# Performance work log

Hardware: AMD Instinct MI355X
Metric: run time of the kernel (lower is better)

Reference implementation:

```python
import jax, jax.numpy as jnp
import numpy as np


def setup_inputs() -> dict:
    key = jax.random.key(0)
    k1, k2 = jax.random.split(key)
    B, H, W, D, C = 2, 128, 128, 128, 4
    image = jax.random.normal(k1, (B, H, W, D, C), dtype=jnp.float32)
    # multiplicative warp field in [0,1) keeps sample coords inside the volume
    transformation = jax.random.uniform(k2, (B, H, W, D, 3), dtype=jnp.float32)
    return {"image": image, "transformation": transformation}


def _make_grid(OH, OW, OD):
    # matches tf.meshgrid(x_lin, y_lin, z_lin) with default 'xy' indexing:
    # each output has shape (OH, OW, OD); stacked last-dim order (x, y, z)
    xl = jnp.linspace(-1.0, 1.0, OW)
    yl = jnp.linspace(-1.0, 1.0, OH)
    zl = jnp.linspace(-1.0, 1.0, OD)
    xc, yc, zc = jnp.meshgrid(xl, yl, zl, indexing="xy")
    return jnp.stack([xc, yc, zc], axis=-1)  # (OH, OW, OD, 3)


def _trilerp_one(img, coords):
    """img: (H, W, D, C); coords: (OH, OW, OD, 3) in [-1, 1]-style space."""
    H, W, D, C = img.shape
    x = 0.5 * (coords[..., 0] + 1.0) * W
    y = 0.5 * (coords[..., 1] + 1.0) * H
    z = 0.5 * (coords[..., 2] + 1.0) * D

    x0 = jnp.floor(x).astype(jnp.int32)
    y0 = jnp.floor(y).astype(jnp.int32)
    z0 = jnp.floor(z).astype(jnp.int32)
    x1 = jnp.clip(x0 + 1, 0, W - 1)
    y1 = jnp.clip(y0 + 1, 0, H - 1)
    z1 = jnp.clip(z0 + 1, 0, D - 1)
    x0 = jnp.clip(x0, 0, W - 1)
    y0 = jnp.clip(y0, 0, H - 1)
    z0 = jnp.clip(z0, 0, D - 1)

    # weights use the CLIPPED upper corners, as in the original
    dx = x1.astype(x.dtype) - x
    dy = y1.astype(y.dtype) - y
    dz = z1.astype(z.dtype) - z

    def g(yy, xx, zz):
        return img[yy, xx, zz]  # (OH, OW, OD, C) gather

    w = lambda a: a[..., None]
    out = (
        w(dz * dx * dy) * g(y0, x0, z0)
        + w(dz * dx * (1 - dy)) * g(y1, x0, z0)
        + w(dz * (1 - dx) * dy) * g(y0, x1, z0)
        + w(dz * (1 - dx) * (1 - dy)) * g(y1, x1, z0)
        + w((1 - dz) * dx * dy) * g(y0, x0, z1)
        + w((1 - dz) * dx * (1 - dy)) * g(y1, x0, z1)
        + w((1 - dz) * (1 - dx) * dy) * g(y0, x1, z1)
        + w((1 - dz) * (1 - dx) * (1 - dy)) * g(y1, x1, z1)
    )
    return out


def reference(image, transformation):
    # image: (B, H, W, D, C); transformation: (B, OH, OW, OD, 3)
    OH, OW, OD = transformation.shape[1:4]
    grid = _make_grid(OH, OW, OD)              # (OH, OW, OD, 3)
    coords = transformation * grid             # elementwise warp, as in source
    return jax.vmap(_trilerp_one, in_axes=(0, 0))(image, coords)
```

## Files before the change

kernel.cpp:

```cpp
#include <hip/hip_runtime.h>
#include <hip/hip_fp16.h>


typedef float f4 __attribute__((ext_vector_type(4)));
typedef unsigned int u32;
typedef u32 u4v __attribute__((ext_vector_type(4), aligned(8)));

__device__ inline float2 h2f(u32 b) {
    __half2 h = __builtin_bit_cast(__half2, b);
    return __half22float2(h);
}
__device__ inline u32 f2h2(float a, float b) {
    __half2 h = __floats2half2_rn(a, b);
    return __builtin_bit_cast(u32, h);
}

__global__ __launch_bounds__(256) void cvtq_kernel(
    const f4* __restrict__ img, u4v* __restrict__ rec, int bb)
{
    int t = blockIdx.x * 256 + threadIdx.x;
    int z = t & 127;
    int x = (t >> 7) & 127;
    int y = t >> 14;
    int x1 = min(x + 1, 127);
    int y1 = min(y + 1, 127);

    f4 v00 = img[bb | (y  << 14) | (x  << 7) | z];
    f4 v10 = img[bb | (y1 << 14) | (x  << 7) | z];
    f4 v01 = img[bb | (y  << 14) | (x1 << 7) | z];
    f4 v11 = img[bb | (y1 << 14) | (x1 << 7) | z];

    int tt = bb | t;

    u4v r0 = { f2h2(v00.x, v00.y), f2h2(v00.z, v00.w),
               f2h2(v10.x, v10.y), f2h2(v10.z, v10.w) };
    u4v r1 = { f2h2(v01.x, v01.y), f2h2(v01.z, v01.w),
               f2h2(v11.x, v11.y), f2h2(v11.z, v11.w) };
    rec[(size_t)tt * 2]     = r0;
    rec[(size_t)tt * 2 + 1] = r1;
}

__global__ __launch_bounds__(256) void st3d_q_kernel(
    const u32* __restrict__ rec,
    const float* __restrict__ trans,
    f4* __restrict__ out,
    int bb)
{
    int bid = blockIdx.x;
    int q   = bid & 7;
    int n   = bid >> 3;
    int mA  = (n << 8) | threadIdx.x;
    int mB  = mA + (1 << 17);

    int qi = (q >> 2) & 1;
    int qj = (q >> 1) & 1;
    int qk = q & 1;

    const float step = 2.0f / 127.0f;

#define SETUPQ(S, mval)                                                    \
    int kp##S  = (mval) & 63;                                              \
    int jp##S  = ((mval) >> 6) & 63;                                       \
    int ip##S  = (mval) >> 12;                                             \
    int ipe##S = qi ? ip##S : (63 - ip##S);      \
    int i##S   = (qi << 6) + ipe##S;                                       \
    int j##S   = (qj << 6) + jp##S;                                        \
    int k##S   = (qk << 6) + kp##S;                                        \
    int idx##S = bb | (i##S << 14) | (j##S << 7) | k##S;                   \
    const float* t##S = trans + (size_t)idx##S * 3;                        \
    float tx##S = __builtin_nontemporal_load(t##S + 0);                    \
    float ty##S = __builtin_nontemporal_load(t##S + 1);                    \
    float tz##S = __builtin_nontemporal_load(t##S + 2);

    SETUPQ(A, mA)
    SETUPQ(B, mB)

#define GATHERQ(S)                                                         \
    float gx##S = -1.0f + step * (float)j##S;                              \
    float gy##S = -1.0f + step * (float)i##S;                              \
    float gz##S = -1.0f + step * (float)k##S;                              \
    float x##S = (tx##S * gx##S + 1.0f) * 64.0f;                           \
    float y##S = (ty##S * gy##S + 1.0f) * 64.0f;                           \
    float z##S = (tz##S * gz##S + 1.0f) * 64.0f;                           \
    int x0##S = (int)floorf(x##S);                                         \
    int y0##S = (int)floorf(y##S);                                         \
    int z0##S = (int)floorf(z##S);                                         \
    int x1##S = min(max(x0##S + 1, 0), 127);                               \
    int y1##S = min(max(y0##S + 1, 0), 127);                               \
    int z1##S = min(max(z0##S + 1, 0), 127);                               \
    x0##S = min(max(x0##S, 0), 127);                                       \
    y0##S = min(max(y0##S, 0), 127);                                       \
    z0##S = min(max(z0##S, 0), 127);                                       \
              \
    float dx##S = (float)x1##S - x##S;                                     \
    float dy##S = (float)y1##S - y##S;                                     \
    float dz##S = (float)z1##S - z##S;                                     \
    int zb##S = min(z0##S, 126);            \
    int i0##S = z0##S - zb##S;             \
    int i1##S = z1##S - zb##S;                             \
    int r##S = bb | (y0##S << 14) | (x0##S << 7) | zb##S;                  \
    const u4v* p##S = (const u4v*)(rec + (size_t)r##S * 8);                \
    u4v L0##S = p##S[0];                       \
    u4v L1##S = p##S[1];                       \
    u4v L2##S = p##S[2];                       \
    u4v L3##S = p##S[3];

    GATHERQ(A)
    GATHERQ(B)

#define ACCQ(lo0, lo1, hi0, hi1, wA, wB)                                   \
    {                                                                      \
        u32 a0 = i0s ? (hi0) : (lo0);                       \
        u32 a1 = i0s ? (hi1) : (lo1);                       \
        u32 b0 = i1s ? (hi0) : (lo0);                       \
        u32 b1 = i1s ? (hi1) : (lo1);                       \
        float2 fa0 = h2f(a0), fa1 = h2f(a1);                               \
        float2 fb0 = h2f(b0), fb1 = h2f(b1);                               \
        ox += (wA) * fa0.x + (wB) * fb0.x;                                 \
        oy += (wA) * fa0.y + (wB) * fb0.y;                                 \
        oz += (wA) * fa1.x + (wB) * fb1.x;                                 \
        ow += (wA) * fa1.y + (wB) * fb1.y;                                 \
    }

#define FINISHQ(S)                                                         \
    {                                                                      \
        float ex = 1.0f - dx##S, ey = 1.0f - dy##S, ez = 1.0f - dz##S;     \
        float wA0 = dz##S * dx##S * dy##S, wB0 = ez * dx##S * dy##S;       \
        float wA1 = dz##S * dx##S * ey,    wB1 = ez * dx##S * ey;          \
        float wA2 = dz##S * ex * dy##S,    wB2 = ez * ex * dy##S;          \
        float wA3 = dz##S * ex * ey,       wB3 = ez * ex * ey;             \
        int i0s = i0##S, i1s = i1##S;                                      \
        float ox = 0.f, oy = 0.f, oz = 0.f, ow = 0.f;                      \
        ACCQ(L0##S.x, L0##S.y, L2##S.x, L2##S.y, wA0, wB0)    \
        ACCQ(L0##S.z, L0##S.w, L2##S.z, L2##S.w, wA1, wB1)    \
        ACCQ(L1##S.x, L1##S.y, L3##S.x, L3##S.y, wA2, wB2)    \
        ACCQ(L1##S.z, L1##S.w, L3##S.z, L3##S.w, wA3, wB3)    \
        f4 o = {ox, oy, oz, ow};                                           \
        __builtin_nontemporal_store(o, &out[idx##S]);                      \
    }

    FINISHQ(A)
    FINISHQ(B)

#undef SETUPQ
#undef GATHERQ
#undef ACCQ
#undef FINISHQ
}

__global__ __launch_bounds__(256) void cvt_kernel(
    const f4* __restrict__ img, uint2* __restrict__ himg)
{
    int idx = blockIdx.x * 256 + threadIdx.x;
    f4 v = img[idx];
    __half2 lo = __floats2half2_rn(v.x, v.y);
    __half2 hi = __floats2half2_rn(v.z, v.w);
    himg[idx] = make_uint2(__builtin_bit_cast(u32, lo), __builtin_bit_cast(u32, hi));
}

__global__ __launch_bounds__(256) void st3d_h_kernel(
    const u32* __restrict__ himg,
    const float* __restrict__ trans,
    f4* __restrict__ out)
{
    int bid = blockIdx.x;
    int q   = bid & 7;
    int n   = bid >> 3;
    int b   = n >> 10;
    int m   = ((n & 1023) << 8) | threadIdx.x;

    int kp = m & 63;
    int jp = (m >> 6) & 63;
    int ip = m >> 12;

    int qi = (q >> 2) & 1;
    int qj = (q >> 1) & 1;
    int qk = q & 1;

    int ipe = qi ? ip : (63 - ip);
    int i = (qi << 6) + ipe;
    int j = (qj << 6) + jp;
    int k = (qk << 6) + kp;

    int idx = (((b << 7) | i) << 14) | (j << 7) | k;

    const float step = 2.0f / 127.0f;
    float gx = -1.0f + step * (float)j;
    float gy = -1.0f + step * (float)i;
    float gz = -1.0f + step * (float)k;

    const float* t = trans + (size_t)idx * 3;
    float tx = __builtin_nontemporal_load(t + 0);
    float ty = __builtin_nontemporal_load(t + 1);
    float tz = __builtin_nontemporal_load(t + 2);

    float x = (tx * gx + 1.0f) * 64.0f;
    float y = (ty * gy + 1.0f) * 64.0f;
    float z = (tz * gz + 1.0f) * 64.0f;

    int x0 = (int)floorf(x);
    int y0 = (int)floorf(y);
    int z0 = (int)floorf(z);
    int x1 = min(max(x0 + 1, 0), 127);
    int y1 = min(max(y0 + 1, 0), 127);
    int z1 = min(max(z0 + 1, 0), 127);
    x0 = min(max(x0, 0), 127);
    y0 = min(max(y0, 0), 127);
    z0 = min(max(z0, 0), 127);

    float dx = (float)x1 - x;
    float dy = (float)y1 - y;
    float dz = (float)z1 - z;
    float ex = 1.0f - dx;
    float ey = 1.0f - dy;
    float ez = 1.0f - dz;

    int zb = min(z0, 126);
    int i0 = z0 - zb;
    int i1 = z1 - zb;

    int bb  = b << 21;
    int ry0 = bb + (y0 << 14);
    int ry1 = bb + (y1 << 14);
    int cx0 = x0 << 7;
    int cx1 = x1 << 7;

    const u4v* p0 = (const u4v*)(himg + (size_t)(ry0 + cx0 + zb) * 2);
    const u4v* p1 = (const u4v*)(himg + (size_t)(ry1 + cx0 + zb) * 2);
    const u4v* p2 = (const u4v*)(himg + (size_t)(ry0 + cx1 + zb) * 2);
    const u4v* p3 = (const u4v*)(himg + (size_t)(ry1 + cx1 + zb) * 2);

    u4v d0 = *p0;
    u4v d1 = *p1;
    u4v d2 = *p2;
    u4v d3 = *p3;

    float wA0 = dz * dx * dy, wB0 = ez * dx * dy;
    float wA1 = dz * dx * ey, wB1 = ez * dx * ey;
    float wA2 = dz * ex * dy, wB2 = ez * ex * dy;
    float wA3 = dz * ex * ey, wB3 = ez * ex * ey;

    float ox = 0.f, oy = 0.f, oz = 0.f, ow = 0.f;

#define ACC(d, wA, wB)                                            \
    {                                                             \
        u32 a0 = i0 ? (d).z : (d).x;                              \
        u32 a1 = i0 ? (d).w : (d).y;                              \
        u32 b0 = i1 ? (d).z : (d).x;                              \
        u32 b1 = i1 ? (d).w : (d).y;                              \
        float2 fa0 = h2f(a0), fa1 = h2f(a1);                      \
        float2 fb0 = h2f(b0), fb1 = h2f(b1);                      \
        ox += (wA) * fa0.x + (wB) * fb0.x;                        \
        oy += (wA) * fa0.y + (wB) * fb0.y;                        \
        oz += (wA) * fa1.x + (wB) * fb1.x;                        \
        ow += (wA) * fa1.y + (wB) * fb1.y;                        \
    }

    ACC(d0, wA0, wB0)
    ACC(d1, wA1, wB1)
    ACC(d2, wA2, wB2)
    ACC(d3, wA3, wB3)
#undef ACC

    f4 o = {ox, oy, oz, ow};
    __builtin_nontemporal_store(o, &out[idx]);
}

__global__ __launch_bounds__(256) void st3d_kernel(
    const float* __restrict__ img,
    const float* __restrict__ trans,
    f4* __restrict__ out)
{
    int bid = blockIdx.x;
    int q   = bid & 7;
    int n   = bid >> 3;
    int b   = n >> 10;
    int m   = ((n & 1023) << 8) | threadIdx.x;

    int kp = m & 63;
    int jp = (m >> 6) & 63;
    int ip = m >> 12;

    int qi = (q >> 2) & 1;
    int qj = (q >> 1) & 1;
    int qk = q & 1;

    int ipe = qi ? ip : (63 - ip);
    int i = (qi << 6) + ipe;
    int j = (qj << 6) + jp;
    int k = (qk << 6) + kp;

    int idx = (((b << 7) | i) << 14) | (j << 7) | k;

    const float step = 2.0f / 127.0f;
    float gx = -1.0f + step * (float)j;
    float gy = -1.0f + step * (float)i;
    float gz = -1.0f + step * (float)k;

    const float* t = trans + (size_t)idx * 3;
    float tx = __builtin_nontemporal_load(t + 0);
    float ty = __builtin_nontemporal_load(t + 1);
    float tz = __builtin_nontemporal_load(t + 2);

    float x = (tx * gx + 1.0f) * 64.0f;
    float y = (ty * gy + 1.0f) * 64.0f;
    float z = (tz * gz + 1.0f) * 64.0f;

    int x0 = (int)floorf(x);
    int y0 = (int)floorf(y);
    int z0 = (int)floorf(z);
    int x1 = min(max(x0 + 1, 0), 127);
    int y1 = min(max(y0 + 1, 0), 127);
    int z1 = min(max(z0 + 1, 0), 127);
    x0 = min(max(x0, 0), 127);
    y0 = min(max(y0, 0), 127);
    z0 = min(max(z0, 0), 127);

    float dx = (float)x1 - x;
    float dy = (float)y1 - y;
    float dz = (float)z1 - z;
    float ex = 1.0f - dx;
    float ey = 1.0f - dy;
    float ez = 1.0f - dz;

    const f4* img4 = (const f4*)img;
    int bb  = b << 21;
    int ry0 = bb + (y0 << 14);
    int ry1 = bb + (y1 << 14);
    int cx0 = x0 << 7;
    int cx1 = x1 << 7;

    int A0 = ry0 + cx0 + z0;
    int A1 = ry1 + cx0 + z0;
    int A2 = ry0 + cx1 + z0;
    int A3 = ry1 + cx1 + z0;
    int dzi = z1 - z0;

    f4 c000 = img4[A0];
    f4 c100 = img4[A1];
    f4 c010 = img4[A2];
    f4 c110 = img4[A3];
    f4 c001 = img4[A0 + dzi];
    f4 c101 = img4[A1 + dzi];
    f4 c011 = img4[A2 + dzi];
    f4 c111 = img4[A3 + dzi];

    float w000 = dz * dx * dy;
    float w100 = dz * dx * ey;
    float w010 = dz * ex * dy;
    float w110 = dz * ex * ey;
    float w001 = ez * dx * dy;
    float w101 = ez * dx * ey;
    float w011 = ez * ex * dy;
    float w111 = ez * ex * ey;

    f4 o = w000*c000 + w100*c100 + w010*c010 + w110*c110
         + w001*c001 + w101*c101 + w011*c011 + w111*c111;

    __builtin_nontemporal_store(o, &out[idx]);
}

extern "C" void kernel_launch(void* const* d_in, const int* in_sizes, int n_in,
                              void* d_out, int out_size, void* d_ws, size_t ws_size,
                              hipStream_t stream) {
    const float* img   = (const float*)d_in[0];
    const float* trans = (const float*)d_in[1];
    f4* out = (f4*)d_out;

    int N = in_sizes[1] / 3;
    int NB = 1 << 21;
    int block = 256;

    size_t need_q = (size_t)N * 32;
    size_t need_h = (size_t)N * 8;

    if (ws_size >= need_q) {
        for (int b = 0; b < 2; ++b) {
            int bb = b << 21;
            cvtq_kernel<<<NB / block, block, 0, stream>>>(
                (const f4*)img, (u4v*)d_ws, bb);
            st3d_q_kernel<<<NB / (2 * block), block, 0, stream>>>(
                (const u32*)d_ws, trans, out, bb);
        }
    } else if (ws_size >= need_h) {
        cvt_kernel<<<N / block, block, 0, stream>>>((const f4*)img, (uint2*)d_ws);
        st3d_h_kernel<<<N / block, block, 0, stream>>>(
            (const u32*)d_ws, trans, out);
    } else {
        st3d_kernel<<<N / block, block, 0, stream>>>(img, trans, out);
    }
}
```

Baseline: 227.9 us.

## Overlap batch-1 conversion with batch-0 sampling in an interleaved fused kernel

Replaces the per-batch sequence of conversion and sampling launches with three launches. The middle kernel interleaves batch-0 trilinear sampling blocks with batch-1 fp16 neighbour-record conversion blocks in a 1:2 ratio, so the memory-bound conversion overlaps the gather-heavy sampling. This removes one launch and one serialization point. The cost is more complex block indexing, and a mixed workload in one kernel may compete for bandwidth and cache.

```diff
diff --git a/kernel.cpp b/kernel.cpp
--- a/kernel.cpp
+++ b/kernel.cpp
@@ -15,10 +15,9 @@
     return __builtin_bit_cast(u32, h);
 }
 
-__global__ __launch_bounds__(256) void cvtq_kernel(
-    const f4* __restrict__ img, u4v* __restrict__ rec, int bb)
-{
-    int t = blockIdx.x * 256 + threadIdx.x;
+__device__ __forceinline__ void cvtq_body(
+    const f4* __restrict__ img, u4v* __restrict__ rec, int bb, int t)
+{
     int z = t & 127;
     int x = (t >> 7) & 127;
     int y = t >> 14;
@@ -40,16 +39,11 @@
     rec[(size_t)tt * 2 + 1] = r1;
 }
 
-__global__ __launch_bounds__(256) void st3d_q_kernel(
-    const u32* __restrict__ rec,
-    const float* __restrict__ trans,
-    f4* __restrict__ out,
-    int bb)
-{
-    int bid = blockIdx.x;
-    int q   = bid & 7;
-    int n   = bid >> 3;
-    int mA  = (n << 8) | threadIdx.x;
+__device__ __forceinline__ void st3d_q_body(
+    const u32* __restrict__ rec, const float* __restrict__ trans,
+    f4* __restrict__ out, int bb, int q, int n, int tid)
+{
+    int mA  = (n << 8) | tid;
     int mB  = mA + (1 << 17);
 
     int qi = (q >> 2) & 1;
@@ -148,6 +142,38 @@
 #undef FINISHQ
 }
 
+__global__ __launch_bounds__(256) void cvtq_kernel(
+    const f4* __restrict__ img, u4v* __restrict__ rec, int bb)
+{
+    cvtq_body(img, rec, bb, blockIdx.x * 256 + threadIdx.x);
+}
+
+__global__ __launch_bounds__(256) void fused_kernel(
+    const f4* __restrict__ img, u4v* __restrict__ rec_w,
+    const u32* __restrict__ rec, const float* __restrict__ trans,
+    f4* __restrict__ out)
+{
+    int bid = blockIdx.x;
+    int d3  = bid / 3;
+    int r3  = bid - d3 * 3;
+    if (r3 == 0) {
+        int q = bid & 7;
+        int n = d3 >> 3;
+        st3d_q_body(rec, trans, out, 0, q, n, threadIdx.x);
+    } else {
+        int cid = 2 * d3 + (r3 - 1);
+        cvtq_body(img, rec_w, 1 << 21, cid * 256 + threadIdx.x);
+    }
+}
+
+__global__ __launch_bounds__(256) void st3d_q_kernel(
+    const u32* __restrict__ rec, const float* __restrict__ trans,
+    f4* __restrict__ out, int bb)
+{
+    int bid = blockIdx.x;
+    st3d_q_body(rec, trans, out, bb, bid & 7, bid >> 3, threadIdx.x);
+}
+
 __global__ __launch_bounds__(256) void cvt_kernel(
     const f4* __restrict__ img, uint2* __restrict__ himg)
 {
@@ -375,13 +401,12 @@
     size_t need_h = (size_t)N * 8;
 
     if (ws_size >= need_q) {
-        for (int b = 0; b < 2; ++b) {
-            int bb = b << 21;
-            cvtq_kernel<<<NB / block, block, 0, stream>>>(
-                (const f4*)img, (u4v*)d_ws, bb);
-            st3d_q_kernel<<<NB / (2 * block), block, 0, stream>>>(
-                (const u32*)d_ws, trans, out, bb);
-        }
+        cvtq_kernel<<<NB / block, block, 0, stream>>>(
+            (const f4*)img, (u4v*)d_ws, 0);
+        fused_kernel<<<3 * (NB / (2 * block)), block, 0, stream>>>(
+            (const f4*)img, (u4v*)d_ws, (const u32*)d_ws, trans, out);
+        st3d_q_kernel<<<NB / (2 * block), block, 0, stream>>>(
+            (const u32*)d_ws, trans, out, NB);
     } else if (ws_size >= need_h) {
         cvt_kernel<<<N / block, block, 0, stream>>>((const f4*)img, (uint2*)d_ws);
         st3d_h_kernel<<<N / block, block, 0, stream>>>(
```

New measurement: 228.7 us. Within noise of the previous version (+0.3%).
